# Optimization experiments

Measured on AMD Instinct MI355X. Metric: run time of the kernel, lower is better.

Reference implementation:

```python
import jax, jax.numpy as jnp
import numpy as np

B, S, E, M = 128, 196, 768, 768

def setup_inputs() -> dict:
    key = jax.random.key(0)
    k1, k2, k3, k4, k5 = jax.random.split(key, 5)
    sent_emb = jax.random.normal(k1, (B, S, E), dtype=jnp.float32)
    # valid event spans: start in [0, S-6), end = start + len, len in [1,5]
    starts = jax.random.randint(k2, (B, 2), 0, S - 6)
    lens = jax.random.randint(k3, (B, 2), 1, 6)
    ends = starts + lens
    batch_e = jnp.stack([starts[:, 0], ends[:, 0], starts[:, 1], ends[:, 1]], axis=1).astype(jnp.int64)
    mlp_w = jax.random.normal(k4, (M, 2 * E), dtype=jnp.float32) * 0.02
    mlp_b = jnp.zeros((M,), dtype=jnp.float32)
    fk_w = jax.random.normal(k5, (M, S * E), dtype=jnp.float32) * 0.005
    fk_b = jnp.zeros((M,), dtype=jnp.float32)
    return {"sent_emb": sent_emb, "batch_e": batch_e, "mlp_w": mlp_w,
            "mlp_b": mlp_b, "fk_w": fk_w, "fk_b": fk_b, "batch_size": B}

def reference(sent_emb, batch_e, mlp_w, mlp_b, fk_w, fk_b, batch_size):
    b, s, e = sent_emb.shape
    # sent_process: flatten each sentence's [S,E] embeddings into one row [S*E]
    sent_emb_cat = sent_emb.reshape(b, s * e)  # [B, S*E]
    # extract_event: mean-pool over the two variable-length spans (vectorized via masks)
    pos = jnp.arange(s)  # [S]
    m1 = ((pos >= batch_e[:, 0:1]) & (pos < batch_e[:, 1:2])).astype(sent_emb.dtype)  # [B,S]
    m2 = ((pos >= batch_e[:, 2:3]) & (pos < batch_e[:, 3:4])).astype(sent_emb.dtype)
    e1 = jnp.einsum('bs,bse->be', m1, sent_emb) / jnp.sum(m1, axis=1, keepdims=True)
    e2 = jnp.einsum('bs,bse->be', m2, sent_emb) / jnp.sum(m2, axis=1, keepdims=True)
    event_pair = jnp.concatenate([e1, e2], axis=1)  # [B, 2E]
    pred = 0.9 * (event_pair @ mlp_w.T + mlp_b) + 0.1 * (sent_emb_cat @ fk_w.T + fk_b)
    return pred
```

## Files before the change

### kernel.cpp

```cpp
#include <hip/hip_runtime.h>
#include <hip/hip_bf16.h>

#define B_ 128
#define S_ 196
#define E_ 768
#define M_ 768
#define KTOT (S_*E_)
#define BK 256
#define SS_TOTAL (KTOT/BK)
#define KSPLIT 32
#define BN 48
#define MTN (M_/BN)
#define PITCH 528
#define ZC 4

typedef __bf16 bf16x8 __attribute__((ext_vector_type(8)));
typedef __bf16 bf16x4 __attribute__((ext_vector_type(4)));
typedef float  f32x4  __attribute__((ext_vector_type(4)));

__device__ inline bf16x8 cvt8(const float* __restrict__ p) {
    float4 a = *(const float4*)p;
    float4 b = *(const float4*)(p + 4);
    bf16x8 r;
    r[0] = (__bf16)a.x; r[1] = (__bf16)a.y; r[2] = (__bf16)a.z; r[3] = (__bf16)a.w;
    r[4] = (__bf16)b.x; r[5] = (__bf16)b.y; r[6] = (__bf16)b.z; r[7] = (__bf16)b.w;
    return r;
}

__device__ inline void barrier_nodrain() {
    asm volatile("s_waitcnt lgkmcnt(0)" ::: "memory");
    __builtin_amdgcn_s_barrier();
}

__global__ void prep(const float* __restrict__ mlp_b,
                     const float* __restrict__ fk_b,
                     const float* __restrict__ A,
                     const int* __restrict__ BE, int be_stride,
                     float* __restrict__ out,
                     float* __restrict__ EP,
                     __bf16* __restrict__ Apk) {
    const int bid = blockIdx.x;
    if (bid < 384) {
        int i = bid * 256 + threadIdx.x;
        int m = i % M_;
        out[i] = 0.9f * mlp_b[m] + 0.1f * fk_b[m];
    } else if (bid < 512) {
        int b = bid - 384;
        int s1 = BE[(b*4 + 0) * be_stride];
        int e1 = BE[(b*4 + 1) * be_stride];
        int s2 = BE[(b*4 + 2) * be_stride];
        int e2 = BE[(b*4 + 3) * be_stride];
        float inv1 = 1.0f / (float)(e1 - s1);
        float inv2 = 1.0f / (float)(e2 - s2);
        for (int c = threadIdx.x; c < E_; c += 256) {
            float sum1 = 0.f, sum2 = 0.f;
            for (int s = s1; s < e1; ++s) sum1 += A[((size_t)b * S_ + s) * E_ + c];
            for (int s = s2; s < e2; ++s) sum2 += A[((size_t)b * S_ + s) * E_ + c];
            EP[b * (2*E_) + c]       = sum1 * inv1;
            EP[b * (2*E_) + E_ + c]  = sum2 * inv2;
        }
    } else {
        const int nchunk = SS_TOTAL * 8 * 8 * 64;
        for (int c = (bid - 512) * 256 + threadIdx.x; c < nchunk; c += 3072 * 256) {
            int lane = c & 63;
            int kf   = (c >> 6) & 7;
            int bt   = (c >> 9) & 7;
            int ss   = c >> 12;
            int b = bt * 16 + (lane & 15);
            int k = ss * BK + kf * 32 + (lane >> 4) * 8;
            *(bf16x8*)(Apk + (size_t)c * 8) = cvt8(A + (size_t)b * KTOT + k);
        }
    }
}


#define LOAD_A(AREG, sl)                                                      \
    _Pragma("unroll")                                                         \
    for (int kf = 0; kf < 8; ++kf)                                            \
        AREG[kf] = *(const bf16x8*)(abase + (size_t)(sl) * 32768 + kf * 512);

#define LOAD_W(sl)                                                            \
    _Pragma("unroll")                                                         \
    for (int i = 0; i < 6; ++i)                                               \
        w[i] = *(const float4*)(wbase + (size_t)i * KTOT + (size_t)(sl) * BK);

#define WRITE_W(buf)                                                          \
    _Pragma("unroll")                                                         \
    for (int i = 0; i < 6; ++i) {                                             \
        bf16x4 h;                                                             \
        h[0] = (__bf16)w[i].x; h[1] = (__bf16)w[i].y;                         \
        h[2] = (__bf16)w[i].z; h[3] = (__bf16)w[i].w;                         \
        *(bf16x4*)(&Wlds[buf][0] + wb + i * PITCH) = h;                       \
    }

#define COMPUTE(AREG, buf)                                                    \
    _Pragma("unroll")                                                         \
    for (int kf = 0; kf < 8; ++kf) {                                          \
        _Pragma("unroll")                                                     \
        for (int n = 0; n < 3; ++n) {                                         \
            bf16x8 wf = *(const bf16x8*)(&Wlds[buf][0] +                      \
                        (n * 16 + r16) * PITCH + kf * 64 + kg * 16);          \
            acc[n] = __builtin_amdgcn_mfma_f32_16x16x32_bf16(AREG[kf], wf,    \
                                                             acc[n], 0, 0, 0);\
        }                                                                     \
    }

__global__ __launch_bounds__(512, 4) void fk_gemm(const __bf16* __restrict__ Apk,
                                                  const float* __restrict__ W,
                                                  float* __restrict__ partial) {
    __shared__ __align__(16) char Wlds[2][BN * PITCH];

    const int wg   = blockIdx.x;
    const int xcd  = wg & 7;
    const int slot = wg >> 3;
    const int kz   = (slot >> 4) * 8 + xcd;
    const int mt   = slot & 15;
    const int ss0 = (SS_TOTAL * kz) / KSPLIT;
    const int SSN = (SS_TOTAL * (kz + 1)) / KSPLIT - ss0;

    const int tid = threadIdx.x;
    const int wv  = tid >> 6;
    const int lane = tid & 63;
    const int r16 = lane & 15;
    const int kg  = lane >> 4;

    const float*  wbase = W + (size_t)(mt * BN + wv * 6) * KTOT
                            + (size_t)ss0 * BK + lane * 4;
    const int     wb    = (wv * 6) * PITCH + lane * 8;
    const __bf16* abase = Apk + ((size_t)ss0 * 8 + wv) * 4096 + lane * 8;

    f32x4 acc[3] = {};
    float4 w[6];
    bf16x8 aA[8], aB[8];

    LOAD_W(0)
    WRITE_W(0)
    LOAD_A(aA, 0)
    LOAD_W(1)
    barrier_nodrain();

    int sl = 0;
    for (; sl + 1 < SSN; sl += 2) {
        LOAD_A(aB, sl + 1)
        COMPUTE(aA, 0)
        WRITE_W(1)
        const bool more2 = (sl + 2 < SSN);
        if (more2) { LOAD_W(sl + 2) }
        barrier_nodrain();
        if (more2) { LOAD_A(aA, sl + 2) }
        COMPUTE(aB, 1)
        if (more2) {
            WRITE_W(0)
            if (sl + 3 < SSN) { LOAD_W(sl + 3) }
            barrier_nodrain();
        }
    }
    if (SSN & 1) {
        COMPUTE(aA, 0)
    }

    float* pz = partial + (size_t)kz * (B_ * M_);
#pragma unroll
    for (int n = 0; n < 3; ++n) {
        const int m = mt * BN + n * 16 + r16;
#pragma unroll
        for (int r = 0; r < 4; ++r) {
            const int b = wv * 16 + kg * 4 + r;
            pz[(size_t)b * M_ + m] = acc[n][r];
        }
    }
}

__global__ __launch_bounds__(256) void post(const float* __restrict__ pp,
                                            const float* __restrict__ EP,
                                            const float* __restrict__ Wm,
                                            float* __restrict__ out) {
    const int bid = blockIdx.x;
    if (bid < 1536) {
        int t = bid * 256 + threadIdx.x;
        int i = t % (B_ * M_);
        int zc = t / (B_ * M_);
        float s = 0.f;
#pragma unroll
        for (int z = zc * (KSPLIT / ZC); z < (zc + 1) * (KSPLIT / ZC); ++z)
            s += pp[(size_t)z * (B_ * M_) + i];
        atomicAdd(out + i, 0.1f * s);
    } else {
        const int wid   = ((bid - 1536) * 256 + threadIdx.x) >> 6;
        const int lane  = threadIdx.x & 63;
        const int bt    = wid & 7;
        const int mt    = wid >> 3;
        const int row16 = lane & 15;
        const int kgrp  = lane >> 4;
        const float* Arow = EP + (size_t)(bt*16 + row16) * (2*E_);
        const float* Brow = Wm + (size_t)(mt*16 + row16) * (2*E_);
        f32x4 acc = {};
        for (int k0 = 0; k0 < 2*E_; k0 += 32) {
            bf16x8 af = cvt8(Arow + k0 + kgrp*8);
            bf16x8 bv = cvt8(Brow + k0 + kgrp*8);
            acc = __builtin_amdgcn_mfma_f32_16x16x32_bf16(af, bv, acc, 0, 0, 0);
        }
        const int m = mt*16 + row16;
#pragma unroll
        for (int r = 0; r < 4; ++r) {
            const int b = bt*16 + kgrp*4 + r;
            atomicAdd(out + b * M_ + m, 0.9f * acc[r]);
        }
    }
}

extern "C" void kernel_launch(void* const* d_in, const int* in_sizes, int n_in,
                              void* d_out, int out_size, void* d_ws, size_t ws_size,
                              hipStream_t stream) {
    const float* se    = (const float*)d_in[0];
    const int*   be    = (const int*)  d_in[1];
    const float* mlp_w = (const float*)d_in[2];
    const float* mlp_b = (const float*)d_in[3];
    const float* fk_w  = (const float*)d_in[4];
    const float* fk_b  = (const float*)d_in[5];
    float* out = (float*)d_out;
    float* ep  = (float*)d_ws;
    float* pp  = ep + (size_t)B_ * 2 * E_;
    __bf16* apk = (__bf16*)(pp + (size_t)KSPLIT * B_ * M_);

    const int be_stride = (in_sizes[1] == B_ * 4 * 2) ? 2 : 1;

    prep<<<3584, 256, 0, stream>>>(mlp_b, fk_b, se, be, be_stride, out, ep, apk);
    fk_gemm<<<MTN * KSPLIT, 512, 0, stream>>>(apk, fk_w, pp);
    post<<<1632, 256, 0, stream>>>(pp, ep, mlp_w, out);
}
```

Measured before the change: 165.8 us.

## Retile fk GEMM to 32x32x16 MFMA with 64-wide N tiles and 40-way K split

The streaming GEMM moves from 16x16x32 MFMA with 48-column tiles and 8 waves to 32x32x16 MFMA with 64-column tiles and 4 waves per block. The split-K factor rises from 32 to 40, and the A pre-pack layout is changed to match the 32-row operand fragments. Wider N tiles mean the packed activations are re-read fewer times across M tiles. In exchange, the A-register double buffering is dropped: each A slice is now loaded right before use, so its global-load latency may be exposed. Fewer threads per block also means less parallelism available to hide the large fp32 weight stream.

```diff
diff --git a/kernel.cpp b/kernel.cpp
--- a/kernel.cpp
+++ b/kernel.cpp
@@ -8,15 +8,16 @@
 #define KTOT (S_*E_)
 #define BK 256
 #define SS_TOTAL (KTOT/BK)
-#define KSPLIT 32
-#define BN 48
+#define KSPLIT 40
+#define BN 64
 #define MTN (M_/BN)
-#define PITCH 528
+#define PITCH 520
 #define ZC 4
 
 typedef __bf16 bf16x8 __attribute__((ext_vector_type(8)));
 typedef __bf16 bf16x4 __attribute__((ext_vector_type(4)));
 typedef float  f32x4  __attribute__((ext_vector_type(4)));
+typedef float  f32x16 __attribute__((ext_vector_type(16)));
 
 __device__ inline bf16x8 cvt8(const float* __restrict__ p) {
     float4 a = *(const float4*)p;
@@ -60,52 +61,60 @@
             EP[b * (2*E_) + E_ + c]  = sum2 * inv2;
         }
     } else {
-        const int nchunk = SS_TOTAL * 8 * 8 * 64;
+        const int nchunk = SS_TOTAL * 4 * 16 * 64;
         for (int c = (bid - 512) * 256 + threadIdx.x; c < nchunk; c += 3072 * 256) {
             int lane = c & 63;
-            int kf   = (c >> 6) & 7;
-            int bt   = (c >> 9) & 7;
+            int kf   = (c >> 6) & 15;
+            int bt   = (c >> 10) & 3;
             int ss   = c >> 12;
-            int b = bt * 16 + (lane & 15);
-            int k = ss * BK + kf * 32 + (lane >> 4) * 8;
+            int b = bt * 32 + (lane & 31);
+            int k = ss * BK + kf * 16 + (lane >> 5) * 8;
             *(bf16x8*)(Apk + (size_t)c * 8) = cvt8(A + (size_t)b * KTOT + k);
         }
     }
 }
 
 
-#define LOAD_A(AREG, sl)                                                      \
+#define LOAD_A(sl)                                                            \
     _Pragma("unroll")                                                         \
-    for (int kf = 0; kf < 8; ++kf)                                            \
-        AREG[kf] = *(const bf16x8*)(abase + (size_t)(sl) * 32768 + kf * 512);
+    for (int kf = 0; kf < 16; ++kf)                                           \
+        aA[kf] = *(const bf16x8*)(abase + (size_t)(sl) * 32768 + kf * 512);
 
 #define LOAD_W(sl)                                                            \
     _Pragma("unroll")                                                         \
-    for (int i = 0; i < 6; ++i)                                               \
+    for (int i = 0; i < 16; ++i)                                              \
         w[i] = *(const float4*)(wbase + (size_t)i * KTOT + (size_t)(sl) * BK);
 
 #define WRITE_W(buf)                                                          \
     _Pragma("unroll")                                                         \
-    for (int i = 0; i < 6; ++i) {                                             \
+    for (int i = 0; i < 16; ++i) {                                            \
         bf16x4 h;                                                             \
         h[0] = (__bf16)w[i].x; h[1] = (__bf16)w[i].y;                         \
         h[2] = (__bf16)w[i].z; h[3] = (__bf16)w[i].w;                         \
         *(bf16x4*)(&Wlds[buf][0] + wb + i * PITCH) = h;                       \
     }
 
-#define COMPUTE(AREG, buf)                                                    \
-    _Pragma("unroll")                                                         \
-    for (int kf = 0; kf < 8; ++kf) {                                          \
+#define COMPUTE(buf)                                                          \
+    {                                                                         \
+        const char* Wb = &Wlds[buf][0];                                       \
         _Pragma("unroll")                                                     \
-        for (int n = 0; n < 3; ++n) {                                         \
-            bf16x8 wf = *(const bf16x8*)(&Wlds[buf][0] +                      \
-                        (n * 16 + r16) * PITCH + kf * 64 + kg * 16);          \
-            acc[n] = __builtin_amdgcn_mfma_f32_16x16x32_bf16(AREG[kf], wf,    \
-                                                             acc[n], 0, 0, 0);\
+        for (int kf = 0; kf < 16; ++kf) {                                     \
+            int off0 = r32 * PITCH + kf * 32 + khalf * 16;                    \
+            bf16x4 lo0 = *(const bf16x4*)(Wb + off0);                         \
+            bf16x4 hi0 = *(const bf16x4*)(Wb + off0 + 8);                     \
+            bf16x8 wf0 = __builtin_shufflevector(lo0, hi0, 0,1,2,3,4,5,6,7);  \
+            acc0 = __builtin_amdgcn_mfma_f32_32x32x16_bf16(aA[kf], wf0,       \
+                                                           acc0, 0, 0, 0);    \
+            int off1 = off0 + 32 * PITCH;                                     \
+            bf16x4 lo1 = *(const bf16x4*)(Wb + off1);                         \
+            bf16x4 hi1 = *(const bf16x4*)(Wb + off1 + 8);                     \
+            bf16x8 wf1 = __builtin_shufflevector(lo1, hi1, 0,1,2,3,4,5,6,7);  \
+            acc1 = __builtin_amdgcn_mfma_f32_32x32x16_bf16(aA[kf], wf1,       \
+                                                           acc1, 0, 0, 0);    \
         }                                                                     \
     }
 
-__global__ __launch_bounds__(512, 4) void fk_gemm(const __bf16* __restrict__ Apk,
+__global__ __launch_bounds__(256, 2) void fk_gemm(const __bf16* __restrict__ Apk,
                                                   const float* __restrict__ W,
                                                   float* __restrict__ partial) {
     __shared__ __align__(16) char Wlds[2][BN * PITCH];
@@ -113,42 +122,41 @@
     const int wg   = blockIdx.x;
     const int xcd  = wg & 7;
     const int slot = wg >> 3;
-    const int kz   = (slot >> 4) * 8 + xcd;
-    const int mt   = slot & 15;
+    const int kz   = (slot / MTN) * 8 + xcd;
+    const int mt   = slot % MTN;
     const int ss0 = (SS_TOTAL * kz) / KSPLIT;
     const int SSN = (SS_TOTAL * (kz + 1)) / KSPLIT - ss0;
 
     const int tid = threadIdx.x;
     const int wv  = tid >> 6;
     const int lane = tid & 63;
-    const int r16 = lane & 15;
-    const int kg  = lane >> 4;
-
-    const float*  wbase = W + (size_t)(mt * BN + wv * 6) * KTOT
+    const int r32 = lane & 31;
+    const int khalf = lane >> 5;
+
+    const float*  wbase = W + (size_t)(mt * BN + wv * 16) * KTOT
                             + (size_t)ss0 * BK + lane * 4;
-    const int     wb    = (wv * 6) * PITCH + lane * 8;
-    const __bf16* abase = Apk + ((size_t)ss0 * 8 + wv) * 4096 + lane * 8;
-
-    f32x4 acc[3] = {};
-    float4 w[6];
-    bf16x8 aA[8], aB[8];
+    const int     wb    = (wv * 16) * PITCH + lane * 8;
+    const __bf16* abase = Apk + ((size_t)ss0 * 4 + wv) * 8192 + lane * 8;
+
+    f32x16 acc0 = {}, acc1 = {};
+    float4 w[16];
+    bf16x8 aA[16];
 
     LOAD_W(0)
     WRITE_W(0)
-    LOAD_A(aA, 0)
     LOAD_W(1)
     barrier_nodrain();
 
     int sl = 0;
     for (; sl + 1 < SSN; sl += 2) {
-        LOAD_A(aB, sl + 1)
-        COMPUTE(aA, 0)
+        LOAD_A(sl)
+        COMPUTE(0)
         WRITE_W(1)
         const bool more2 = (sl + 2 < SSN);
         if (more2) { LOAD_W(sl + 2) }
         barrier_nodrain();
-        if (more2) { LOAD_A(aA, sl + 2) }
-        COMPUTE(aB, 1)
+        LOAD_A(sl + 1)
+        COMPUTE(1)
         if (more2) {
             WRITE_W(0)
             if (sl + 3 < SSN) { LOAD_W(sl + 3) }
@@ -156,18 +164,16 @@
         }
     }
     if (SSN & 1) {
-        COMPUTE(aA, 0)
+        LOAD_A(sl)
+        COMPUTE(0)
     }
 
     float* pz = partial + (size_t)kz * (B_ * M_);
 #pragma unroll
-    for (int n = 0; n < 3; ++n) {
-        const int m = mt * BN + n * 16 + r16;
-#pragma unroll
-        for (int r = 0; r < 4; ++r) {
-            const int b = wv * 16 + kg * 4 + r;
-            pz[(size_t)b * M_ + m] = acc[n][r];
-        }
+    for (int reg = 0; reg < 16; ++reg) {
+        const int b = wv * 32 + (reg & 3) + 8 * (reg >> 2) + 4 * khalf;
+        pz[(size_t)b * M_ + mt * BN + r32]      = acc0[reg];
+        pz[(size_t)b * M_ + mt * BN + 32 + r32] = acc1[reg];
     }
 }
 
@@ -226,6 +232,6 @@
     const int be_stride = (in_sizes[1] == B_ * 4 * 2) ? 2 : 1;
 
     prep<<<3584, 256, 0, stream>>>(mlp_b, fk_b, se, be, be_stride, out, ep, apk);
-    fk_gemm<<<MTN * KSPLIT, 512, 0, stream>>>(apk, fk_w, pp);
+    fk_gemm<<<MTN * KSPLIT, 256, 0, stream>>>(apk, fk_w, pp);
     post<<<1632, 256, 0, stream>>>(pp, ep, mlp_w, out);
 }
```

New measurement: 181.8 us. +9.7%, slower.

## Give each fk_gemm wave two batch tiles and raise the K-split to 48

Applied to the files above, without the earlier changes.

Each fk_gemm wave now computes two 16-row batch tiles against the same LDS weight fragment, halving LDS reads per MFMA. Workgroups shrink to 256 threads that each stage 12 weight rows, and the K dimension is split 48 ways instead of 32 to keep the grid size up. The A fragments are no longer prefetched one stage ahead; they are loaded right before use. This exposes global/L2 latency and lowers the number of resident waves per CU, while adding more partial-sum traffic for the reduction kernel.

```diff
diff --git a/kernel.cpp b/kernel.cpp
--- a/kernel.cpp
+++ b/kernel.cpp
@@ -8,7 +8,7 @@
 #define KTOT (S_*E_)
 #define BK 256
 #define SS_TOTAL (KTOT/BK)
-#define KSPLIT 32
+#define KSPLIT 48
 #define BN 48
 #define MTN (M_/BN)
 #define PITCH 528
@@ -74,38 +74,42 @@
 }
 
 
-#define LOAD_A(AREG, sl)                                                      \
-    _Pragma("unroll")                                                         \
-    for (int kf = 0; kf < 8; ++kf)                                            \
-        AREG[kf] = *(const bf16x8*)(abase + (size_t)(sl) * 32768 + kf * 512);
+#define LOAD_A(sl)                                                            \
+    _Pragma("unroll")                                                         \
+    for (int kf = 0; kf < 8; ++kf) {                                          \
+        aT0[kf] = *(const bf16x8*)(abase0 + (size_t)(sl) * 32768 + kf * 512); \
+        aT1[kf] = *(const bf16x8*)(abase1 + (size_t)(sl) * 32768 + kf * 512); \
+    }
 
 #define LOAD_W(sl)                                                            \
     _Pragma("unroll")                                                         \
-    for (int i = 0; i < 6; ++i)                                               \
+    for (int i = 0; i < 12; ++i)                                              \
         w[i] = *(const float4*)(wbase + (size_t)i * KTOT + (size_t)(sl) * BK);
 
 #define WRITE_W(buf)                                                          \
     _Pragma("unroll")                                                         \
-    for (int i = 0; i < 6; ++i) {                                             \
+    for (int i = 0; i < 12; ++i) {                                            \
         bf16x4 h;                                                             \
         h[0] = (__bf16)w[i].x; h[1] = (__bf16)w[i].y;                         \
         h[2] = (__bf16)w[i].z; h[3] = (__bf16)w[i].w;                         \
         *(bf16x4*)(&Wlds[buf][0] + wb + i * PITCH) = h;                       \
     }
 
-#define COMPUTE(AREG, buf)                                                    \
+#define COMPUTE(buf)                                                          \
     _Pragma("unroll")                                                         \
     for (int kf = 0; kf < 8; ++kf) {                                          \
         _Pragma("unroll")                                                     \
         for (int n = 0; n < 3; ++n) {                                         \
             bf16x8 wf = *(const bf16x8*)(&Wlds[buf][0] +                      \
                         (n * 16 + r16) * PITCH + kf * 64 + kg * 16);          \
-            acc[n] = __builtin_amdgcn_mfma_f32_16x16x32_bf16(AREG[kf], wf,    \
-                                                             acc[n], 0, 0, 0);\
+            acc0[n] = __builtin_amdgcn_mfma_f32_16x16x32_bf16(aT0[kf], wf,    \
+                                                              acc0[n], 0,0,0);\
+            acc1[n] = __builtin_amdgcn_mfma_f32_16x16x32_bf16(aT1[kf], wf,    \
+                                                              acc1[n], 0,0,0);\
         }                                                                     \
     }
 
-__global__ __launch_bounds__(512, 4) void fk_gemm(const __bf16* __restrict__ Apk,
+__global__ __launch_bounds__(256, 3) void fk_gemm(const __bf16* __restrict__ Apk,
                                                   const float* __restrict__ W,
                                                   float* __restrict__ partial) {
     __shared__ __align__(16) char Wlds[2][BN * PITCH];
@@ -124,31 +128,31 @@
     const int r16 = lane & 15;
     const int kg  = lane >> 4;
 
-    const float*  wbase = W + (size_t)(mt * BN + wv * 6) * KTOT
+    const float*  wbase = W + (size_t)(mt * BN + wv * 12) * KTOT
                             + (size_t)ss0 * BK + lane * 4;
-    const int     wb    = (wv * 6) * PITCH + lane * 8;
-    const __bf16* abase = Apk + ((size_t)ss0 * 8 + wv) * 4096 + lane * 8;
-
-    f32x4 acc[3] = {};
-    float4 w[6];
-    bf16x8 aA[8], aB[8];
+    const int     wb    = (wv * 12) * PITCH + lane * 8;
+    const __bf16* abase0 = Apk + ((size_t)ss0 * 8 + 2 * wv)     * 4096 + lane * 8;
+    const __bf16* abase1 = Apk + ((size_t)ss0 * 8 + 2 * wv + 1) * 4096 + lane * 8;
+
+    f32x4 acc0[3] = {}, acc1[3] = {};
+    float4 w[12];
+    bf16x8 aT0[8], aT1[8];
 
     LOAD_W(0)
     WRITE_W(0)
-    LOAD_A(aA, 0)
     LOAD_W(1)
     barrier_nodrain();
 
     int sl = 0;
     for (; sl + 1 < SSN; sl += 2) {
-        LOAD_A(aB, sl + 1)
-        COMPUTE(aA, 0)
+        LOAD_A(sl)
+        COMPUTE(0)
         WRITE_W(1)
         const bool more2 = (sl + 2 < SSN);
         if (more2) { LOAD_W(sl + 2) }
         barrier_nodrain();
-        if (more2) { LOAD_A(aA, sl + 2) }
-        COMPUTE(aB, 1)
+        LOAD_A(sl + 1)
+        COMPUTE(1)
         if (more2) {
             WRITE_W(0)
             if (sl + 3 < SSN) { LOAD_W(sl + 3) }
@@ -156,7 +160,8 @@
         }
     }
     if (SSN & 1) {
-        COMPUTE(aA, 0)
+        LOAD_A(sl)
+        COMPUTE(0)
     }
 
     float* pz = partial + (size_t)kz * (B_ * M_);
@@ -165,8 +170,9 @@
         const int m = mt * BN + n * 16 + r16;
 #pragma unroll
         for (int r = 0; r < 4; ++r) {
-            const int b = wv * 16 + kg * 4 + r;
-            pz[(size_t)b * M_ + m] = acc[n][r];
+            const int b0 = (2 * wv) * 16 + kg * 4 + r;
+            pz[(size_t)b0 * M_ + m]        = acc0[n][r];
+            pz[(size_t)(b0 + 16) * M_ + m] = acc1[n][r];
         }
     }
 }
@@ -226,6 +232,6 @@
     const int be_stride = (in_sizes[1] == B_ * 4 * 2) ? 2 : 1;
 
     prep<<<3584, 256, 0, stream>>>(mlp_b, fk_b, se, be, be_stride, out, ep, apk);
-    fk_gemm<<<MTN * KSPLIT, 512, 0, stream>>>(apk, fk_w, pp);
+    fk_gemm<<<MTN * KSPLIT, 256, 0, stream>>>(apk, fk_w, pp);
     post<<<1632, 256, 0, stream>>>(pp, ep, mlp_w, out);
 }
```

Result: slower. 172.1 us (+3.8%).

## Stream fp32 weights directly into LDS via global_load_lds with XOR swizzle

Applied to the files above, without the earlier changes.

The weight tile now goes straight from global memory into swizzled LDS through `global_load_lds`, still in fp32. It is converted to bf16 only when the MFMA operands are read, which removes the register staging and convert-and-store pass. The K step is halved to 128 to fit fp32 rows in LDS, the A operand is no longer double-buffered in registers, and the pipeline is simplified to one barrier per step with a full vmcnt drain. The cost is doubled LDS read traffic, more conversions in the inner loop, and A-load and drain latency that is less hidden.

```diff
diff --git a/kernel.cpp b/kernel.cpp
--- a/kernel.cpp
+++ b/kernel.cpp
@@ -6,16 +6,14 @@
 #define E_ 768
 #define M_ 768
 #define KTOT (S_*E_)
-#define BK 256
+#define BK 128
 #define SS_TOTAL (KTOT/BK)
 #define KSPLIT 32
 #define BN 48
 #define MTN (M_/BN)
-#define PITCH 528
 #define ZC 4
 
 typedef __bf16 bf16x8 __attribute__((ext_vector_type(8)));
-typedef __bf16 bf16x4 __attribute__((ext_vector_type(4)));
 typedef float  f32x4  __attribute__((ext_vector_type(4)));
 
 __device__ inline bf16x8 cvt8(const float* __restrict__ p) {
@@ -27,7 +25,21 @@
     return r;
 }
 
-__device__ inline void barrier_nodrain() {
+__device__ inline bf16x8 cvt8v(float4 a, float4 b) {
+    bf16x8 r;
+    r[0] = (__bf16)a.x; r[1] = (__bf16)a.y; r[2] = (__bf16)a.z; r[3] = (__bf16)a.w;
+    r[4] = (__bf16)b.x; r[5] = (__bf16)b.y; r[6] = (__bf16)b.z; r[7] = (__bf16)b.w;
+    return r;
+}
+
+__device__ inline void gload16(const float* g, void* l) {
+    __builtin_amdgcn_global_load_lds(
+        (const __attribute__((address_space(1))) void*)g,
+        (__attribute__((address_space(3))) void*)l, 16, 0, 0);
+}
+
+__device__ inline void wait_and_barrier() {
+    asm volatile("s_waitcnt vmcnt(0)" ::: "memory");
     asm volatile("s_waitcnt lgkmcnt(0)" ::: "memory");
     __builtin_amdgcn_s_barrier();
 }
@@ -60,12 +72,12 @@
             EP[b * (2*E_) + E_ + c]  = sum2 * inv2;
         }
     } else {
-        const int nchunk = SS_TOTAL * 8 * 8 * 64;
+        const int nchunk = SS_TOTAL * 8 * 4 * 64;
         for (int c = (bid - 512) * 256 + threadIdx.x; c < nchunk; c += 3072 * 256) {
             int lane = c & 63;
-            int kf   = (c >> 6) & 7;
-            int bt   = (c >> 9) & 7;
-            int ss   = c >> 12;
+            int kf   = (c >> 6) & 3;
+            int bt   = (c >> 8) & 7;
+            int ss   = c >> 11;
             int b = bt * 16 + (lane & 15);
             int k = ss * BK + kf * 32 + (lane >> 4) * 8;
             *(bf16x8*)(Apk + (size_t)c * 8) = cvt8(A + (size_t)b * KTOT + k);
@@ -74,33 +86,32 @@
 }
 
 
-#define LOAD_A(AREG, sl)                                                      \
+#define ISSUE_W(sl, bb)                                                       \
     _Pragma("unroll")                                                         \
-    for (int kf = 0; kf < 8; ++kf)                                            \
-        AREG[kf] = *(const bf16x8*)(abase + (size_t)(sl) * 32768 + kf * 512);
-
-#define LOAD_W(sl)                                                            \
+    for (int j = 0; j < 3; ++j) {                                             \
+        const int row = wv * 6 + 2 * j + (lane >> 5);                         \
+        const float* g = W + (size_t)(mt * BN + row) * KTOT                   \
+                         + (size_t)(ss0 + (sl)) * BK                          \
+                         + (((((lane & 31) * 16) ^ ((row & 7) << 4))) >> 2);  \
+        gload16(g, &Wlds[bb][(wv * 6 + 2 * j) * 512]);                        \
+    }
+
+#define LOAD_A(sl)                                                            \
     _Pragma("unroll")                                                         \
-    for (int i = 0; i < 6; ++i)                                               \
-        w[i] = *(const float4*)(wbase + (size_t)i * KTOT + (size_t)(sl) * BK);
-
-#define WRITE_W(buf)                                                          \
+    for (int kf = 0; kf < 4; ++kf)                                            \
+        aA[kf] = *(const bf16x8*)(abase + (size_t)(sl) * 16384 + kf * 512);
+
+#define COMPUTE(bb)                                                           \
     _Pragma("unroll")                                                         \
-    for (int i = 0; i < 6; ++i) {                                             \
-        bf16x4 h;                                                             \
-        h[0] = (__bf16)w[i].x; h[1] = (__bf16)w[i].y;                         \
-        h[2] = (__bf16)w[i].z; h[3] = (__bf16)w[i].w;                         \
-        *(bf16x4*)(&Wlds[buf][0] + wb + i * PITCH) = h;                       \
-    }
-
-#define COMPUTE(AREG, buf)                                                    \
-    _Pragma("unroll")                                                         \
-    for (int kf = 0; kf < 8; ++kf) {                                          \
+    for (int kf = 0; kf < 4; ++kf) {                                          \
         _Pragma("unroll")                                                     \
         for (int n = 0; n < 3; ++n) {                                         \
-            bf16x8 wf = *(const bf16x8*)(&Wlds[buf][0] +                      \
-                        (n * 16 + r16) * PITCH + kf * 64 + kg * 16);          \
-            acc[n] = __builtin_amdgcn_mfma_f32_16x16x32_bf16(AREG[kf], wf,    \
+            const char* p = &Wlds[bb][(n * 16 + r16) * 512];                  \
+            const int cb = kf * 128 + kg * 32;                                \
+            float4 f0 = *(const float4*)(p + ((cb) ^ sw));                    \
+            float4 f1 = *(const float4*)(p + ((cb + 16) ^ sw));               \
+            bf16x8 wf = cvt8v(f0, f1);                                        \
+            acc[n] = __builtin_amdgcn_mfma_f32_16x16x32_bf16(aA[kf], wf,      \
                                                              acc[n], 0, 0, 0);\
         }                                                                     \
     }
@@ -108,7 +119,7 @@
 __global__ __launch_bounds__(512, 4) void fk_gemm(const __bf16* __restrict__ Apk,
                                                   const float* __restrict__ W,
                                                   float* __restrict__ partial) {
-    __shared__ __align__(16) char Wlds[2][BN * PITCH];
+    __shared__ __align__(16) char Wlds[2][BN * 512];
 
     const int wg   = blockIdx.x;
     const int xcd  = wg & 7;
@@ -123,40 +134,22 @@
     const int lane = tid & 63;
     const int r16 = lane & 15;
     const int kg  = lane >> 4;
-
-    const float*  wbase = W + (size_t)(mt * BN + wv * 6) * KTOT
-                            + (size_t)ss0 * BK + lane * 4;
-    const int     wb    = (wv * 6) * PITCH + lane * 8;
-    const __bf16* abase = Apk + ((size_t)ss0 * 8 + wv) * 4096 + lane * 8;
+    const int sw  = (r16 & 7) << 4;
+
+    const __bf16* abase = Apk + ((size_t)ss0 * 8 + wv) * 2048 + lane * 8;
 
     f32x4 acc[3] = {};
-    float4 w[6];
-    bf16x8 aA[8], aB[8];
-
-    LOAD_W(0)
-    WRITE_W(0)
-    LOAD_A(aA, 0)
-    LOAD_W(1)
-    barrier_nodrain();
-
-    int sl = 0;
-    for (; sl + 1 < SSN; sl += 2) {
-        LOAD_A(aB, sl + 1)
-        COMPUTE(aA, 0)
-        WRITE_W(1)
-        const bool more2 = (sl + 2 < SSN);
-        if (more2) { LOAD_W(sl + 2) }
-        barrier_nodrain();
-        if (more2) { LOAD_A(aA, sl + 2) }
-        COMPUTE(aB, 1)
-        if (more2) {
-            WRITE_W(0)
-            if (sl + 3 < SSN) { LOAD_W(sl + 3) }
-            barrier_nodrain();
-        }
-    }
-    if (SSN & 1) {
-        COMPUTE(aA, 0)
+    bf16x8 aA[4];
+
+    ISSUE_W(0, 0)
+
+    int bcur = 0;
+    for (int sl = 0; sl < SSN; ++sl) {
+        wait_and_barrier();
+        if (sl + 1 < SSN) { ISSUE_W(sl + 1, bcur ^ 1) }
+        LOAD_A(sl)
+        COMPUTE(bcur)
+        bcur ^= 1;
     }
 
     float* pz = partial + (size_t)kz * (B_ * M_);
```

Measured after the change: 177.1 us. +6.8%, slower.
